# Kernel tuning notes

Measured on AMD Instinct MI355X. Metric: run time of the kernel, lower is better.

## Reference

```python
import jax, jax.numpy as jnp
import numpy as np

N = 100000   # nodes
E = 1600000  # edges
F_IN, H1, H2, C = 22, 128, 256, 4


def spmm(edge_src, edge_dst, edge_w, X):
    # A @ X where A is sparse (COO): out[d] = sum_{e: dst[e]=d} w[e] * X[src[e]]
    msgs = X[edge_src] * edge_w[:, None]          # [E, F]
    return jax.ops.segment_sum(msgs, edge_dst, num_segments=N)


def setup_inputs() -> dict:
    key = jax.random.key(0)
    ks = jax.random.split(key, 10)
    x = jax.random.normal(ks[0], (N, F_IN), dtype=jnp.float32)
    edge_src = jax.random.randint(ks[1], (E,), 0, N, dtype=jnp.int32)
    edge_dst = jax.random.randint(ks[2], (E,), 0, N, dtype=jnp.int32)
    edge_w = jax.random.uniform(ks[3], (E,), dtype=jnp.float32)
    s1 = 1.0 / np.sqrt(H1)
    s2 = 1.0 / np.sqrt(H2)
    W1 = jax.random.uniform(ks[4], (F_IN, H1), jnp.float32, -s1, s1)
    b1 = jax.random.uniform(ks[5], (H1,), jnp.float32, -s1, s1)
    W2 = jax.random.uniform(ks[6], (H1, H2), jnp.float32, -s2, s2)
    b2 = jax.random.uniform(ks[7], (H2,), jnp.float32, -s2, s2)
    Wm = jax.random.normal(ks[8], (H2, C), dtype=jnp.float32) * 0.05
    bm = jnp.zeros((C,), dtype=jnp.float32)
    return {"x": x, "edge_src": edge_src, "edge_dst": edge_dst, "edge_w": edge_w,
            "W1": W1, "b1": b1, "W2": W2, "b2": b2, "Wm": Wm, "bm": bm}


def reference(x, edge_src, edge_dst, edge_w, W1, b1, W2, b2, Wm, bm):
    # Layer 1: relu(A @ (X @ W1) + b1)
    h = jax.nn.relu(spmm(edge_src, edge_dst, edge_w, x @ W1) + b1)
    # dropout is a no-op in eval mode
    # Layer 2: A @ (h @ W2) + b2
    h = spmm(edge_src, edge_dst, edge_w, h @ W2) + b2
    # MLP head: Linear(256,4) + LogSoftmax(dim=1)
    return jax.nn.log_softmax(h @ Wm + bm, axis=-1)
```

## Files before the change

### kernel.cpp

```cpp
#include <hip/hip_runtime.h>

#define N_NODES 100000
#define N_EDGES 1600000
#define F_IN 22
#define H1 128
#define H2 256
#define C_OUT 4

#define W_SCALE 32767.0f
#define W_INV   (1.0f / 32767.0f)

#define BSHIFT 9
#define NBUCK 196
#define CHUNK 5000
#define NBLK_A 320
#define BCAP 12288
#define BSLACK 3584

__global__ __launch_bounds__(256) void xb_k(
    const float* __restrict__ x, unsigned* __restrict__ xb)
{
    int i = blockIdx.x * 256 + threadIdx.x;
    if (i >= N_NODES * 11) return;
    int n = i / 11, p = i - n * 11;
    unsigned u0 = __float_as_uint(x[n * F_IN + 2 * p]);
    unsigned u1 = __float_as_uint(x[n * F_IN + 2 * p + 1]);
    u0 = (u0 + 0x7fffu + ((u0 >> 16) & 1u)) >> 16;
    u1 = (u1 + 0x7fffu + ((u1 >> 16) & 1u)) >> 16;
    xb[i] = u0 | (u1 << 16);
}

__global__ __launch_bounds__(256) void binA_k(
    const int* __restrict__ esrc, const int* __restrict__ edst,
    const float* __restrict__ ew, int* __restrict__ bcnt,
    uint2* __restrict__ binned)
{
    __shared__ int l_base[NBUCK];
    __shared__ int l_cnt[NBUCK];
    int t = threadIdx.x;
    int e0 = blockIdx.x * CHUNK;

    for (int i = t; i < NBUCK; i += 256) l_cnt[i] = 0;
    __syncthreads();
    for (int i = t; i < CHUNK; i += 256)
        atomicAdd(&l_cnt[edst[e0 + i] >> BSHIFT], 1);
    __syncthreads();
    for (int i = t; i < NBUCK; i += 256) {
        int c = l_cnt[i];
        l_base[i] = c ? atomicAdd(&bcnt[i], c) : 0;
    }
    __syncthreads();
    for (int i = t; i < NBUCK; i += 256) l_cnt[i] = 0;
    __syncthreads();
    for (int i = t; i < CHUNK; i += 256) {
        int e = e0 + i;
        int d = edst[e];
        int b = d >> BSHIFT;
        int off = l_base[b] + atomicAdd(&l_cnt[b], 1);
        int wq = (int)(ew[e] * W_SCALE + 0.5f);
        wq = wq > 32767 ? 32767 : wq;
        unsigned rec = ((unsigned)esrc[e] << 15) | (unsigned)wq;
        if (off < BCAP)
            binned[(size_t)b * BCAP + off] = make_uint2(rec, (unsigned)(d & 511));
    }
}

__global__ __launch_bounds__(256) void scanB_k(
    const int* __restrict__ bcnt, int* __restrict__ bbase)
{
    int t = threadIdx.x;
    int v = (t < NBUCK) ? (bcnt[t] + BSLACK) : 0;
    __shared__ int sA[256], sB[256];
    sA[t] = v; __syncthreads();
    int* src = sA; int* dst = sB;
    for (int off = 1; off < 256; off <<= 1) {
        dst[t] = src[t] + (t >= off ? src[t - off] : 0);
        __syncthreads();
        int* tmp = src; src = dst; dst = tmp;
    }
    if (t < NBUCK) bbase[t] = (t > 0) ? src[t - 1] : 0;
}

__global__ __launch_bounds__(512) void binB_k(
    const uint2* __restrict__ binned, const int* __restrict__ bcnt,
    const int* __restrict__ bbase, int* __restrict__ rowbeg,
    int* __restrict__ rowend, unsigned* __restrict__ rec_s)
{
    __shared__ int l_hist[512];
    __shared__ int sA[512], sB[512];
    __shared__ int l_cur[512];
    __shared__ unsigned l_out[BCAP];
    int b = blockIdx.x;
    int t = threadIdx.x;
    int node0 = b << BSHIFT;
    int base = bbase[b];
    int cnt = min(bcnt[b], BCAP);
    const uint2* reg = binned + (size_t)b * BCAP;

    l_hist[t] = 0;
    __syncthreads();
    for (int i = t; i < cnt; i += 512)
        atomicAdd(&l_hist[reg[i].y], 1);
    __syncthreads();
    int pc = (l_hist[t] + 7) & ~7;
    sA[t] = pc; __syncthreads();
    int* src = sA; int* dst = sB;
    for (int off = 1; off < 512; off <<= 1) {
        dst[t] = src[t] + (t >= off ? src[t - off] : 0);
        __syncthreads();
        int* tmp = src; src = dst; dst = tmp;
    }
    int excl = (t > 0) ? src[t - 1] : 0;
    int ptot = src[511];
    int node = node0 + t;
    if (node < N_NODES) {
        rowbeg[node] = base + excl;
        rowend[node] = base + excl + pc;
    }
    l_cur[t] = excl;
    __syncthreads();
    for (int i = t; i < ptot; i += 512) l_out[i] = 0;
    __syncthreads();
    for (int i = t; i < cnt; i += 512) {
        uint2 r = reg[i];
        int p = atomicAdd(&l_cur[r.y], 1);
        l_out[p] = r.x;
    }
    __syncthreads();
    for (int i = t; i < ptot; i += 512)
        rec_s[base + i] = l_out[i];
}

__global__ __launch_bounds__(512) void wf_k(
    const float* __restrict__ W2, const float* __restrict__ Wm,
    const float* __restrict__ b2, const float* __restrict__ bm,
    float* __restrict__ Wf, float* __restrict__ bhead)
{
    int tid = threadIdx.x;
    int k = tid >> 2, c = tid & 3;
    float acc = 0.f;
    for (int j = 0; j < H2; ++j)
        acc = fmaf(W2[k * H2 + j], Wm[j * C_OUT + c], acc);
    Wf[k * C_OUT + c] = acc;
    if (tid < C_OUT) {
        float a = bm[tid];
        for (int j = 0; j < H2; ++j)
            a = fmaf(b2[j], Wm[j * C_OUT + tid], a);
        bhead[tid] = a;
    }
}

__global__ __launch_bounds__(256) void layer1z_k(
    const unsigned* __restrict__ xb,
    const int* __restrict__ rowbeg,
    const int* __restrict__ rowend,
    const unsigned* __restrict__ rec,
    const float* __restrict__ W1,
    const float* __restrict__ b1,
    const float* __restrict__ Wf,
    float4* __restrict__ z)
{
    __shared__ float4 ws1[F_IN * 32];
    __shared__ float4 wsf[H1];
    __shared__ float ys[8][24];
    int tid = threadIdx.x;
    int g = tid >> 5, lane = tid & 31;
    int d = blockIdx.x * 8 + g;
    int beg = rowbeg[d], end = rowend[d];

    for (int i = tid; i < F_IN * 32; i += 256) ws1[i] = ((const float4*)W1)[i];
    if (tid < H1) wsf[tid] = ((const float4*)Wf)[tid];

    int l2 = lane < 22 ? lane : 21;
    int eslot = l2 >= 11;
    int pair = l2 - 11 * eslot;

    float aA0 = 0.f, aA1 = 0.f, aA2 = 0.f, aA3 = 0.f;
    float aB0 = 0.f, aB1 = 0.f, aB2 = 0.f, aB3 = 0.f;
    for (int j = beg; j < end; j += 8) {
        unsigned q0 = rec[j + 0 + eslot];
        unsigned q1 = rec[j + 2 + eslot];
        unsigned q2 = rec[j + 4 + eslot];
        unsigned q3 = rec[j + 6 + eslot];
        float w0 = (float)(q0 & 0x7fffu) * W_INV;
        float w1 = (float)(q1 & 0x7fffu) * W_INV;
        float w2 = (float)(q2 & 0x7fffu) * W_INV;
        float w3 = (float)(q3 & 0x7fffu) * W_INV;
        unsigned x0 = xb[(size_t)(q0 >> 15) * 11 + pair];
        unsigned x1 = xb[(size_t)(q1 >> 15) * 11 + pair];
        unsigned x2 = xb[(size_t)(q2 >> 15) * 11 + pair];
        unsigned x3 = xb[(size_t)(q3 >> 15) * 11 + pair];
        aA0 = fmaf(w0, __uint_as_float(x0 << 16), aA0);
        aB0 = fmaf(w0, __uint_as_float(x0 & 0xFFFF0000u), aB0);
        aA1 = fmaf(w1, __uint_as_float(x1 << 16), aA1);
        aB1 = fmaf(w1, __uint_as_float(x1 & 0xFFFF0000u), aB1);
        aA2 = fmaf(w2, __uint_as_float(x2 << 16), aA2);
        aB2 = fmaf(w2, __uint_as_float(x2 & 0xFFFF0000u), aB2);
        aA3 = fmaf(w3, __uint_as_float(x3 << 16), aA3);
        aB3 = fmaf(w3, __uint_as_float(x3 & 0xFFFF0000u), aB3);
    }
    float sA = (aA0 + aA1) + (aA2 + aA3);
    float sB = (aB0 + aB1) + (aB2 + aB3);
    float oA = __shfl(sA, 11 + pair, 32);
    float oB = __shfl(sB, 11 + pair, 32);
    if (lane < 11) {
        ys[g][2 * pair]     = sA + oA;
        ys[g][2 * pair + 1] = sB + oB;
    }
    __syncthreads();

    float4 a = ((const float4*)b1)[lane];
#pragma unroll
    for (int k = 0; k < F_IN; ++k) {
        float y = ys[g][k];
        float4 w = ws1[k * 32 + lane];
        a.x = fmaf(y, w.x, a.x);
        a.y = fmaf(y, w.y, a.y);
        a.z = fmaf(y, w.z, a.z);
        a.w = fmaf(y, w.w, a.w);
    }
    a.x = a.x > 0.f ? a.x : 0.f;
    a.y = a.y > 0.f ? a.y : 0.f;
    a.z = a.z > 0.f ? a.z : 0.f;
    a.w = a.w > 0.f ? a.w : 0.f;

    float av[4] = {a.x, a.y, a.z, a.w};
    float pl[4] = {0.f, 0.f, 0.f, 0.f};
#pragma unroll
    for (int r = 0; r < 4; ++r) {
        float4 w = wsf[lane * 4 + r];
        pl[0] = fmaf(av[r], w.x, pl[0]);
        pl[1] = fmaf(av[r], w.y, pl[1]);
        pl[2] = fmaf(av[r], w.z, pl[2]);
        pl[3] = fmaf(av[r], w.w, pl[3]);
    }
#pragma unroll
    for (int mask = 16; mask >= 1; mask >>= 1) {
#pragma unroll
        for (int c = 0; c < 4; ++c)
            pl[c] += __shfl_xor(pl[c], mask, 64);
    }
    if (lane == 0)
        z[d] = make_float4(pl[0], pl[1], pl[2], pl[3]);
}

__global__ __launch_bounds__(256) void agg4_k(
    const float4* __restrict__ z,
    const int* __restrict__ rowbeg,
    const int* __restrict__ rowend,
    const unsigned* __restrict__ rec,
    const float* __restrict__ bhead,
    float* __restrict__ out)
{
    int tid = threadIdx.x;
    int g = tid >> 3, sub = tid & 7;
    int d = blockIdx.x * 32 + g;
    int beg = rowbeg[d], end = rowend[d];

    float4 acc = {0.f, 0.f, 0.f, 0.f};
    for (int j = beg + sub; j < end; j += 8) {
        unsigned r = rec[j];
        float w = (float)(r & 0x7fffu) * W_INV;
        float4 v = z[r >> 15];
        acc.x = fmaf(w, v.x, acc.x);
        acc.y = fmaf(w, v.y, acc.y);
        acc.z = fmaf(w, v.z, acc.z);
        acc.w = fmaf(w, v.w, acc.w);
    }
#pragma unroll
    for (int mask = 4; mask >= 1; mask >>= 1) {
        acc.x += __shfl_xor(acc.x, mask, 64);
        acc.y += __shfl_xor(acc.y, mask, 64);
        acc.z += __shfl_xor(acc.z, mask, 64);
        acc.w += __shfl_xor(acc.w, mask, 64);
    }
    if (sub == 0) {
        float l0 = acc.x + bhead[0];
        float l1 = acc.y + bhead[1];
        float l2 = acc.z + bhead[2];
        float l3 = acc.w + bhead[3];
        float mx = fmaxf(fmaxf(l0, l1), fmaxf(l2, l3));
        float s = expf(l0 - mx) + expf(l1 - mx) + expf(l2 - mx) + expf(l3 - mx);
        float lg = mx + logf(s);
        ((float4*)out)[d] = make_float4(l0 - lg, l1 - lg, l2 - lg, l3 - lg);
    }
}

extern "C" void kernel_launch(void* const* d_in, const int* in_sizes, int n_in,
                              void* d_out, int out_size, void* d_ws, size_t ws_size,
                              hipStream_t stream) {
    const float* x    = (const float*)d_in[0];
    const int*   esrc = (const int*)d_in[1];
    const int*   edst = (const int*)d_in[2];
    const float* ew   = (const float*)d_in[3];
    const float* W1   = (const float*)d_in[4];
    const float* b1   = (const float*)d_in[5];
    const float* W2   = (const float*)d_in[6];
    const float* b2   = (const float*)d_in[7];
    const float* Wm   = (const float*)d_in[8];
    const float* bm   = (const float*)d_in[9];
    float* out = (float*)d_out;

    char* ws = (char*)d_ws;
    float4*   z      = (float4*)ws;   ws += (size_t)N_NODES * 16;
    uint2*    binned = (uint2*)ws;    ws += (size_t)NBUCK * BCAP * 8;
    unsigned* rec_s  = (unsigned*)ws; ws += (size_t)(N_EDGES + NBUCK * BSLACK) * 4;
    unsigned* xb     = (unsigned*)ws; ws += (size_t)N_NODES * 11 * 4;
    int*      rowbeg = (int*)ws;      ws += (size_t)N_NODES * 4;
    int*      rowend = (int*)ws;      ws += (size_t)N_NODES * 4;
    int*      bcnt   = (int*)ws;      ws += NBUCK * 4;
    int*      bbase  = (int*)ws;      ws += NBUCK * 4;
    float*    Wf     = (float*)ws;    ws += H1 * C_OUT * 4;
    float*    bhead  = (float*)ws;    ws += C_OUT * 4;

    xb_k<<<(N_NODES * 11 + 255) / 256, 256, 0, stream>>>(x, xb);

    hipMemsetAsync(bcnt, 0, NBUCK * 4, stream);
    binA_k <<<NBLK_A, 256, 0, stream>>>(esrc, edst, ew, bcnt, binned);
    scanB_k<<<1, 256, 0, stream>>>(bcnt, bbase);
    binB_k <<<NBUCK, 512, 0, stream>>>(binned, bcnt, bbase, rowbeg, rowend, rec_s);

    wf_k<<<1, 512, 0, stream>>>(W2, Wm, b2, bm, Wf, bhead);

    layer1z_k<<<N_NODES / 8, 256, 0, stream>>>(xb, rowbeg, rowend, rec_s, W1, b1, Wf, z);
    agg4_k<<<N_NODES / 32, 256, 0, stream>>>(z, rowbeg, rowend, rec_s, bhead, out);
}
```

Before: 126.8 us.

## Fuse small setup kernels and stage edge records in LDS during binning

Merges the bf16 packing of x into the binning kernel as extra blocks, and merges the bucket scan with the W2·Wm fold into one two-block launch. This cuts two kernel launches and lets independent work overlap. The binning pass now reads each edge once into shared memory instead of re-reading dst, src and weight from global memory, with a smaller chunk size and a bounds check on the last chunk. The layer-1 W1 tile is re-laid out in LDS as scalar planes instead of float4 rows, which changes the bank access pattern. The costs are higher LDS use per binning block (32 KB) and heterogeneous blocks within one grid.

Measured after the change: 159.0 us. 25.4% more time.

```diff
diff --git a/kernel.cpp b/kernel.cpp
--- a/kernel.cpp
+++ b/kernel.cpp
@@ -12,38 +12,51 @@
 
 #define BSHIFT 9
 #define NBUCK 196
-#define CHUNK 5000
-#define NBLK_A 320
+#define CHUNK 4096
+#define NBLK_A 391
 #define BCAP 12288
 #define BSLACK 3584
-
-__global__ __launch_bounds__(256) void xb_k(
-    const float* __restrict__ x, unsigned* __restrict__ xb)
-{
-    int i = blockIdx.x * 256 + threadIdx.x;
-    if (i >= N_NODES * 11) return;
-    int n = i / 11, p = i - n * 11;
-    unsigned u0 = __float_as_uint(x[n * F_IN + 2 * p]);
-    unsigned u1 = __float_as_uint(x[n * F_IN + 2 * p + 1]);
-    u0 = (u0 + 0x7fffu + ((u0 >> 16) & 1u)) >> 16;
-    u1 = (u1 + 0x7fffu + ((u1 >> 16) & 1u)) >> 16;
-    xb[i] = u0 | (u1 << 16);
-}
-
-__global__ __launch_bounds__(256) void binA_k(
+#define XB_BLOCKS 4297
+
+__global__ __launch_bounds__(256) void binA_xb_k(
     const int* __restrict__ esrc, const int* __restrict__ edst,
     const float* __restrict__ ew, int* __restrict__ bcnt,
-    uint2* __restrict__ binned)
-{
+    uint2* __restrict__ binned,
+    const float* __restrict__ x, unsigned* __restrict__ xb)
+{
+    __shared__ uint2 l_rec[CHUNK];
     __shared__ int l_base[NBUCK];
     __shared__ int l_cnt[NBUCK];
     int t = threadIdx.x;
-    int e0 = blockIdx.x * CHUNK;
+    int bid = blockIdx.x;
+
+    if (bid >= NBLK_A) {
+        int i = (bid - NBLK_A) * 256 + t;
+        if (i < N_NODES * 11) {
+            int n = i / 11, p = i - n * 11;
+            unsigned u0 = __float_as_uint(x[n * F_IN + 2 * p]);
+            unsigned u1 = __float_as_uint(x[n * F_IN + 2 * p + 1]);
+            u0 = (u0 + 0x7fffu + ((u0 >> 16) & 1u)) >> 16;
+            u1 = (u1 + 0x7fffu + ((u1 >> 16) & 1u)) >> 16;
+            xb[i] = u0 | (u1 << 16);
+        }
+        return;
+    }
+
+    int e0 = bid * CHUNK;
+    int n = min(CHUNK, N_EDGES - e0);
 
     for (int i = t; i < NBUCK; i += 256) l_cnt[i] = 0;
     __syncthreads();
-    for (int i = t; i < CHUNK; i += 256)
-        atomicAdd(&l_cnt[edst[e0 + i] >> BSHIFT], 1);
+    for (int i = t; i < n; i += 256) {
+        int e = e0 + i;
+        int d = edst[e];
+        int wq = (int)(ew[e] * W_SCALE + 0.5f);
+        wq = wq > 32767 ? 32767 : wq;
+        unsigned rec = ((unsigned)esrc[e] << 15) | (unsigned)wq;
+        l_rec[i] = make_uint2(rec, (unsigned)d);
+        atomicAdd(&l_cnt[d >> BSHIFT], 1);
+    }
     __syncthreads();
     for (int i = t; i < NBUCK; i += 256) {
         int c = l_cnt[i];
@@ -52,33 +65,47 @@
     __syncthreads();
     for (int i = t; i < NBUCK; i += 256) l_cnt[i] = 0;
     __syncthreads();
-    for (int i = t; i < CHUNK; i += 256) {
-        int e = e0 + i;
-        int d = edst[e];
+    for (int i = t; i < n; i += 256) {
+        uint2 r = l_rec[i];
+        int d = (int)r.y;
         int b = d >> BSHIFT;
         int off = l_base[b] + atomicAdd(&l_cnt[b], 1);
-        int wq = (int)(ew[e] * W_SCALE + 0.5f);
-        wq = wq > 32767 ? 32767 : wq;
-        unsigned rec = ((unsigned)esrc[e] << 15) | (unsigned)wq;
         if (off < BCAP)
-            binned[(size_t)b * BCAP + off] = make_uint2(rec, (unsigned)(d & 511));
-    }
-}
-
-__global__ __launch_bounds__(256) void scanB_k(
-    const int* __restrict__ bcnt, int* __restrict__ bbase)
+            binned[(size_t)b * BCAP + off] = make_uint2(r.x, (unsigned)(d & 511));
+    }
+}
+
+__global__ __launch_bounds__(512) void scanB_wf_k(
+    const int* __restrict__ bcnt, int* __restrict__ bbase,
+    const float* __restrict__ W2, const float* __restrict__ Wm,
+    const float* __restrict__ b2, const float* __restrict__ bm,
+    float* __restrict__ Wf, float* __restrict__ bhead)
 {
     int t = threadIdx.x;
-    int v = (t < NBUCK) ? (bcnt[t] + BSLACK) : 0;
-    __shared__ int sA[256], sB[256];
-    sA[t] = v; __syncthreads();
-    int* src = sA; int* dst = sB;
-    for (int off = 1; off < 256; off <<= 1) {
-        dst[t] = src[t] + (t >= off ? src[t - off] : 0);
-        __syncthreads();
-        int* tmp = src; src = dst; dst = tmp;
-    }
-    if (t < NBUCK) bbase[t] = (t > 0) ? src[t - 1] : 0;
+    if (blockIdx.x == 0) {
+        __shared__ int sA[512], sB[512];
+        int v = (t < NBUCK) ? (bcnt[t] + BSLACK) : 0;
+        sA[t] = v; __syncthreads();
+        int* src = sA; int* dst = sB;
+        for (int off = 1; off < 512; off <<= 1) {
+            dst[t] = src[t] + (t >= off ? src[t - off] : 0);
+            __syncthreads();
+            int* tmp = src; src = dst; dst = tmp;
+        }
+        if (t < NBUCK) bbase[t] = (t > 0) ? src[t - 1] : 0;
+    } else {
+        int k = t >> 2, c = t & 3;
+        float acc = 0.f;
+        for (int j = 0; j < H2; ++j)
+            acc = fmaf(W2[k * H2 + j], Wm[j * C_OUT + c], acc);
+        Wf[k * C_OUT + c] = acc;
+        if (t < C_OUT) {
+            float a = bm[t];
+            for (int j = 0; j < H2; ++j)
+                a = fmaf(b2[j], Wm[j * C_OUT + t], a);
+            bhead[t] = a;
+        }
+    }
 }
 
 __global__ __launch_bounds__(512) void binB_k(
@@ -131,25 +158,6 @@
         rec_s[base + i] = l_out[i];
 }
 
-__global__ __launch_bounds__(512) void wf_k(
-    const float* __restrict__ W2, const float* __restrict__ Wm,
-    const float* __restrict__ b2, const float* __restrict__ bm,
-    float* __restrict__ Wf, float* __restrict__ bhead)
-{
-    int tid = threadIdx.x;
-    int k = tid >> 2, c = tid & 3;
-    float acc = 0.f;
-    for (int j = 0; j < H2; ++j)
-        acc = fmaf(W2[k * H2 + j], Wm[j * C_OUT + c], acc);
-    Wf[k * C_OUT + c] = acc;
-    if (tid < C_OUT) {
-        float a = bm[tid];
-        for (int j = 0; j < H2; ++j)
-            a = fmaf(b2[j], Wm[j * C_OUT + tid], a);
-        bhead[tid] = a;
-    }
-}
-
 __global__ __launch_bounds__(256) void layer1z_k(
     const unsigned* __restrict__ xb,
     const int* __restrict__ rowbeg,
@@ -160,7 +168,7 @@
     const float* __restrict__ Wf,
     float4* __restrict__ z)
 {
-    __shared__ float4 ws1[F_IN * 32];
+    __shared__ float ws1f[F_IN * 128];
     __shared__ float4 wsf[H1];
     __shared__ float ys[8][24];
     int tid = threadIdx.x;
@@ -168,7 +176,10 @@
     int d = blockIdx.x * 8 + g;
     int beg = rowbeg[d], end = rowend[d];
 
-    for (int i = tid; i < F_IN * 32; i += 256) ws1[i] = ((const float4*)W1)[i];
+    for (int i = tid; i < F_IN * 128; i += 256) {
+        int k = i >> 7, r = i & 127, j = r >> 5, l = r & 31;
+        ws1f[i] = W1[(k << 7) + (l << 2) + j];
+    }
     if (tid < H1) wsf[tid] = ((const float4*)Wf)[tid];
 
     int l2 = lane < 22 ? lane : 21;
@@ -213,11 +224,10 @@
 #pragma unroll
     for (int k = 0; k < F_IN; ++k) {
         float y = ys[g][k];
-        float4 w = ws1[k * 32 + lane];
-        a.x = fmaf(y, w.x, a.x);
-        a.y = fmaf(y, w.y, a.y);
-        a.z = fmaf(y, w.z, a.z);
-        a.w = fmaf(y, w.w, a.w);
+        a.x = fmaf(y, ws1f[k * 128 + lane], a.x);
+        a.y = fmaf(y, ws1f[k * 128 + 32 + lane], a.y);
+        a.z = fmaf(y, ws1f[k * 128 + 64 + lane], a.z);
+        a.w = fmaf(y, ws1f[k * 128 + 96 + lane], a.w);
     }
     a.x = a.x > 0.f ? a.x : 0.f;
     a.y = a.y > 0.f ? a.y : 0.f;
@@ -313,14 +323,13 @@
     float*    Wf     = (float*)ws;    ws += H1 * C_OUT * 4;
     float*    bhead  = (float*)ws;    ws += C_OUT * 4;
 
-    xb_k<<<(N_NODES * 11 + 255) / 256, 256, 0, stream>>>(x, xb);
-
     hipMemsetAsync(bcnt, 0, NBUCK * 4, stream);
-    binA_k <<<NBLK_A, 256, 0, stream>>>(esrc, edst, ew, bcnt, binned);
-    scanB_k<<<1, 256, 0, stream>>>(bcnt, bbase);
-    binB_k <<<NBUCK, 512, 0, stream>>>(binned, bcnt, bbase, rowbeg, rowend, rec_s);
-
-    wf_k<<<1, 512, 0, stream>>>(W2, Wm, b2, bm, Wf, bhead);
+    binA_xb_k<<<NBLK_A + XB_BLOCKS, 256, 0, stream>>>(
+        esrc, edst, ew, bcnt, binned, x, xb);
+
+    scanB_wf_k<<<2, 512, 0, stream>>>(bcnt, bbase, W2, Wm, b2, bm, Wf, bhead);
+
+    binB_k<<<NBUCK, 512, 0, stream>>>(binned, bcnt, bbase, rowbeg, rowend, rec_s);
 
     layer1z_k<<<N_NODES / 8, 256, 0, stream>>>(xb, rowbeg, rowend, rec_s, W1, b1, Wf, z);
     agg4_k<<<N_NODES / 32, 256, 0, stream>>>(z, rowbeg, rowend, rec_s, bhead, out);
```
